# Kernel tuning notes

Hardware: AMD Instinct MI355X
Metric: run time of the kernel (lower is better)

Reference implementation:

```python
import jax, jax.numpy as jnp
import numpy as np

N, D, I, O = 4096, 64, 512, 512  # samples, node_nums (bases), input_size, output_size


def setup_inputs() -> dict:
    key = jax.random.key(0)
    k1, k2, k3, k4 = jax.random.split(key, 4)
    # xavier_uniform bounds
    w_bound = float(np.sqrt(6.0 / (I + O)))
    b_bound = float(np.sqrt(6.0 / (D + O)))
    return {
        "x": jax.random.normal(k1, (N, I), dtype=jnp.float32),
        "var_vector": jax.random.uniform(k2, (N, D), dtype=jnp.float32),
        "W_1": jax.random.uniform(k3, (D, I, O), dtype=jnp.float32, minval=-w_bound, maxval=w_bound),
        "b_1": jax.random.uniform(k4, (D, O), dtype=jnp.float32, minval=-b_bound, maxval=b_bound),
    }


def reference(x, var_vector, W_1, b_1):
    # Math identical to: einsum('nd,dio->nio') then bmm(x[:,None,:], W)[:,0,:] + b.
    # Reordered contraction: contract x against each basis first (never forms n,i,o).
    y = jnp.einsum('ni,dio->ndo', x, W_1)        # [n, d, o]
    out = jnp.einsum('nd,ndo->no', var_vector, y)  # [n, o]
    b = jnp.einsum('nd,do->no', var_vector, b_1)   # [n, o]
    return out + b
```

## Files before the change

kernel.cpp:

```cpp
#include <hip/hip_runtime.h>
#include <hip/hip_bf16.h>
#include <stdint.h>
#include <stddef.h>

#define N_ 4096
#define D_ 64
#define I_ 512
#define O_ 512

#define BM 128
#define BN 128
#define BK 64
#define SPLITS 4
#define DPG (D_ / SPLITS)
#define KSTEPS (I_ / BK)
#define NSTEP (DPG * KSTEPS)

typedef float  floatx4 __attribute__((ext_vector_type(4)));
typedef short  shortx8 __attribute__((ext_vector_type(8)));

__device__ __forceinline__ void gload_lds16(const void* g, void* l) {
  __builtin_amdgcn_global_load_lds(
      (const __attribute__((address_space(1))) void*)g,
      (__attribute__((address_space(3))) void*)l, 16, 0, 0);
}

__device__ __forceinline__ unsigned short f2bf(float f) {
  union { float f; unsigned int u; } c; c.f = f;
  unsigned int u = c.u;
  return (unsigned short)((u + 0x7fffu + ((u >> 16) & 1u)) >> 16);
}

__device__ __forceinline__ void mfma_bf16(floatx4& c, shortx8 a, shortx8 b) {
  asm("v_mfma_f32_16x16x32_bf16 %0, %1, %2, %0" : "+v"(c) : "v"(a), "v"(b));
}

__global__ void k_cvt_x(const float* __restrict__ x, unsigned short* __restrict__ xb) {
  int idx = (blockIdx.x * blockDim.x + threadIdx.x) * 8;
  floatx4 a = *(const floatx4*)(x + idx);
  floatx4 b = *(const floatx4*)(x + idx + 4);
  shortx8 o;
  o[0] = (short)f2bf(a[0]); o[1] = (short)f2bf(a[1]);
  o[2] = (short)f2bf(a[2]); o[3] = (short)f2bf(a[3]);
  o[4] = (short)f2bf(b[0]); o[5] = (short)f2bf(b[1]);
  o[6] = (short)f2bf(b[2]); o[7] = (short)f2bf(b[3]);
  *(shortx8*)(xb + idx) = o;
}

__global__ void k_cvt_w(const float* __restrict__ w, unsigned short* __restrict__ wt) {
  __shared__ unsigned short T[64][72];
  int bid = blockIdx.x;
  int d  = bid >> 6;
  int it = (bid >> 3) & 7;
  int ot = bid & 7;
  int i0 = it * 64, o0 = ot * 64;
  int t = threadIdx.x;
  const float* wp = w + ((size_t)d * I_ + i0) * O_ + o0;
  #pragma unroll
  for (int j = 0; j < 16; ++j) {
    int idx = j * 256 + t;
    int r = idx >> 6, c = idx & 63;
    T[r][c] = f2bf(wp[(size_t)r * O_ + c]);
  }
  __syncthreads();
  unsigned short* op = wt + ((size_t)d * O_ + o0) * I_ + i0;
  #pragma unroll
  for (int j = 0; j < 16; ++j) {
    int idx = j * 256 + t;
    int r = idx >> 6, c = idx & 63;
    op[(size_t)r * I_ + c] = T[c][r];
  }
}

__global__ void k_bias(const float* __restrict__ var, const float* __restrict__ b1,
                       float* __restrict__ out) {
  __shared__ float vs[16][64];
  int n0 = blockIdx.x * 16;
  int t = threadIdx.x;
  #pragma unroll
  for (int j = 0; j < 4; ++j) {
    int idx = j * 256 + t;
    vs[idx >> 6][idx & 63] = var[(size_t)n0 * D_ + idx];
  }
  __syncthreads();
  float a0[16], a1[16];
  #pragma unroll
  for (int r = 0; r < 16; ++r) { a0[r] = 0.f; a1[r] = 0.f; }
  for (int d = 0; d < D_; ++d) {
    float b0 = b1[(size_t)d * O_ + t];
    float bb = b1[(size_t)d * O_ + 256 + t];
    #pragma unroll
    for (int r = 0; r < 16; ++r) { a0[r] += vs[r][d] * b0; a1[r] += vs[r][d] * bb; }
  }
  #pragma unroll
  for (int r = 0; r < 16; ++r) {
    out[(size_t)(n0 + r) * O_ + t]       = a0[r];
    out[(size_t)(n0 + r) * O_ + 256 + t] = a1[r];
  }
}

__global__ __launch_bounds__(256, 2) void k_gemm(
    const unsigned short* __restrict__ xb, const unsigned short* __restrict__ wt,
    const float* __restrict__ var, float* __restrict__ out) {
  __shared__ alignas(16) unsigned short lA[2][BM * BK];
  __shared__ alignas(16) unsigned short lB[2][BN * BK];
  __shared__ alignas(16) float lV[DPG * BM];

  const int tid = threadIdx.x;
  const int bx  = blockIdx.x;
  const int split = bx & (SPLITS - 1);
  const int tile  = bx >> 2;
  const int ot = tile & 3;
  const int mt = tile >> 2;
  const int brow = mt * BM, bcol = ot * BN, d0 = split * DPG;

  const int lane = tid & 63, wid = tid >> 6;
  const int wr = wid >> 1, wc = wid & 1;
  const int l15 = lane & 15, l4 = lane >> 4;

  #pragma unroll
  for (int j = 0; j < (DPG * BM) / 256; ++j) {
    int idx = j * 256 + tid;
    int dd = idx >> 7, row = idx & (BM - 1);
    lV[idx] = var[(size_t)(brow + row) * D_ + d0 + dd];
  }

  const floatx4 vzero = {0.f, 0.f, 0.f, 0.f};
  floatx4 master[4][4];
  #pragma unroll
  for (int m = 0; m < 4; ++m)
    #pragma unroll
    for (int n = 0; n < 4; ++n) master[m][n] = vzero;
  floatx4 accd[4][4];

  auto stage = [&](int s, int buf) {
    const int d  = d0 + (s >> 3);
    const int kk = s & 7;
    const char* xsrc = (const char*)xb + ((size_t)brow * I_ + (size_t)kk * BK) * 2;
    const char* wsrc = (const char*)wt + (((size_t)d * O_ + bcol) * I_ + (size_t)kk * BK) * 2;
    char* la = (char*)&lA[buf][0];
    char* lb = (char*)&lB[buf][0];
    #pragma unroll
    for (int c = 0; c < 4; ++c) {
      int chunk = c * 256 + tid;
      int p = chunk << 4;
      int row = p >> 7;
      int colG = (p & 127) ^ ((row & 7) << 4);
      gload_lds16(xsrc + (size_t)row * (I_ * 2) + colG, la + p);
      gload_lds16(wsrc + (size_t)row * (I_ * 2) + colG, lb + p);
    }
  };

  stage(0, 0);

  int s = 0;
  for (int dl = 0; dl < DPG; ++dl) {
    #pragma unroll
    for (int m = 0; m < 4; ++m)
      #pragma unroll
      for (int n = 0; n < 4; ++n) accd[m][n] = vzero;

    for (int kk = 0; kk < KSTEPS; ++kk, ++s) {
      const int buf = s & 1;
      __syncthreads();
      if (s + 1 < NSTEP) stage(s + 1, buf ^ 1);
      #pragma unroll
      for (int ks = 0; ks < 2; ++ks) {
        shortx8 av[4], bv[4];
        #pragma unroll
        for (int m = 0; m < 4; ++m) {
          int row = wr * 64 + m * 16 + l15;
          int cb = ks * 64 + l4 * 16;
          av[m] = *(const shortx8*)((const char*)&lA[buf][0] + row * 128 +
                                    (cb ^ ((row & 7) << 4)));
        }
        #pragma unroll
        for (int n = 0; n < 4; ++n) {
          int row = wc * 64 + n * 16 + l15;
          int cb = ks * 64 + l4 * 16;
          bv[n] = *(const shortx8*)((const char*)&lB[buf][0] + row * 128 +
                                    (cb ^ ((row & 7) << 4)));
        }
        #pragma unroll
        for (int m = 0; m < 4; ++m)
          #pragma unroll
          for (int n = 0; n < 4; ++n)
            mfma_bf16(accd[m][n], av[m], bv[n]);
      }
    }

    #pragma unroll
    for (int m = 0; m < 4; ++m) {
      floatx4 vv = *(const floatx4*)&lV[dl * BM + wr * 64 + m * 16 + l4 * 4];
      #pragma unroll
      for (int n = 0; n < 4; ++n)
        #pragma unroll
        for (int r = 0; r < 4; ++r)
          master[m][n][r] += vv[r] * accd[m][n][r];
    }
  }

  #pragma unroll
  for (int m = 0; m < 4; ++m) {
    int row0 = brow + wr * 64 + m * 16 + l4 * 4;
    #pragma unroll
    for (int n = 0; n < 4; ++n) {
      int col = bcol + wc * 64 + n * 16 + l15;
      #pragma unroll
      for (int r = 0; r < 4; ++r)
        atomicAdd(out + (size_t)(row0 + r) * O_ + col, master[m][n][r]);
    }
  }
}

__global__ void k_naive(const float* __restrict__ x, const float* __restrict__ var,
                        const float* __restrict__ w, const float* __restrict__ b1,
                        float* __restrict__ out) {
  int n = blockIdx.x;
  int o = blockIdx.y * 128 + threadIdx.x;
  const float* xp = x + (size_t)n * I_;
  float acc = 0.f;
  for (int d = 0; d < D_; ++d) {
    const float* wp = w + (size_t)d * I_ * O_ + o;
    float y = 0.f;
    for (int i = 0; i < I_; ++i) y += xp[i] * wp[(size_t)i * O_];
    acc += var[(size_t)n * D_ + d] * (y + b1[(size_t)d * O_ + o]);
  }
  out[(size_t)n * O_ + o] = acc;
}

extern "C" void kernel_launch(void* const* d_in, const int* in_sizes, int n_in,
                              void* d_out, int out_size, void* d_ws, size_t ws_size,
                              hipStream_t stream) {
  const float* x   = (const float*)d_in[0];
  const float* var = (const float*)d_in[1];
  const float* W   = (const float*)d_in[2];
  const float* b1  = (const float*)d_in[3];
  float* out = (float*)d_out;

  const size_t wt_bytes = (size_t)D_ * I_ * O_ * 2;
  const size_t xb_bytes = (size_t)N_ * I_ * 2;
  if (ws_size >= wt_bytes + xb_bytes) {
    unsigned short* wt = (unsigned short*)d_ws;
    unsigned short* xb = (unsigned short*)((char*)d_ws + wt_bytes);
    k_cvt_x<<<dim3((N_ * I_) / (256 * 8)), dim3(256), 0, stream>>>(x, xb);
    k_cvt_w<<<dim3(D_ * 64), dim3(256), 0, stream>>>(W, wt);
    k_bias<<<dim3(N_ / 16), dim3(256), 0, stream>>>(var, b1, out);
    k_gemm<<<dim3((N_ / BM) * (O_ / BN) * SPLITS), dim3(256), 0, stream>>>(xb, wt, var, out);
  } else {
    k_naive<<<dim3(N_, O_ / 128), dim3(128), 0, stream>>>(x, var, W, b1, out);
  }
}
```

Baseline: 197.0 us.

## Enlarge GEMM tile to 256 rows and process basis pairs per A tile

Doubles the row tile to 256 and uses 512-thread blocks. Each loaded x tile is reused against two basis weight tiles per k-step, with two accumulator sets merged into the master sum using their var coefficients. This cuts A-tile reloads and halves the number of pipeline steps. The leading per-step __syncthreads is replaced by a per-thread vmcnt wait plus a trailing s_barrier, and MFMA priority is raised with s_setprio. Risks: no block-wide barrier separates the async LDS loads from reads of other threads' data, larger LDS use limits occupancy to one block per CU, and a meaningless no-op edit appears in the fallback kernel.

```diff
diff --git a/kernel.cpp b/kernel.cpp
--- a/kernel.cpp
+++ b/kernel.cpp
@@ -8,13 +8,14 @@
 #define I_ 512
 #define O_ 512
 
-#define BM 128
+#define BM 256
 #define BN 128
 #define BK 64
 #define SPLITS 4
-#define DPG (D_ / SPLITS)
+#define DPG 16
+#define PAIRS (DPG / 2)
 #define KSTEPS (I_ / BK)
-#define NSTEP (DPG * KSTEPS)
+#define NSTEP (PAIRS * KSTEPS)
 
 typedef float  floatx4 __attribute__((ext_vector_type(4)));
 typedef short  shortx8 __attribute__((ext_vector_type(8)));
@@ -99,19 +100,18 @@
   }
 }
 
-__global__ __launch_bounds__(256, 2) void k_gemm(
+__global__ __launch_bounds__(512, 2) void k_gemm(
     const unsigned short* __restrict__ xb, const unsigned short* __restrict__ wt,
     const float* __restrict__ var, float* __restrict__ out) {
   __shared__ alignas(16) unsigned short lA[2][BM * BK];
-  __shared__ alignas(16) unsigned short lB[2][BN * BK];
+  __shared__ alignas(16) unsigned short lB[2][2][BN * BK];
   __shared__ alignas(16) float lV[DPG * BM];
 
   const int tid = threadIdx.x;
-  const int bx  = blockIdx.x;
-  const int split = bx & (SPLITS - 1);
-  const int tile  = bx >> 2;
-  const int ot = tile & 3;
-  const int mt = tile >> 2;
+  const int bid = blockIdx.x;
+  const int g  = bid & 15;
+  const int mt = bid >> 4;
+  const int ot = g >> 2, split = g & 3;
   const int brow = mt * BM, bcol = ot * BN, d0 = split * DPG;
 
   const int lane = tid & 63, wid = tid >> 6;
@@ -119,11 +119,40 @@
   const int l15 = lane & 15, l4 = lane >> 4;
 
   #pragma unroll
-  for (int j = 0; j < (DPG * BM) / 256; ++j) {
-    int idx = j * 256 + tid;
-    int dd = idx >> 7, row = idx & (BM - 1);
+  for (int j = 0; j < (DPG * BM) / 512; ++j) {
+    int idx = j * 512 + tid;
+    int dd = idx >> 8, row = idx & (BM - 1);
     lV[idx] = var[(size_t)(brow + row) * D_ + d0 + dd];
   }
+
+  auto stage = [&](int s, int buf) {
+    const int p  = s >> 3;
+    const int kk = s & 7;
+    const int da = d0 + 2 * p;
+    const char* xsrc = (const char*)xb + ((size_t)brow * I_ + (size_t)kk * BK) * 2;
+    const char* w0 = (const char*)wt + (((size_t)da * O_ + bcol) * I_ + (size_t)kk * BK) * 2;
+    const char* w1 = (const char*)wt + (((size_t)(da + 1) * O_ + bcol) * I_ + (size_t)kk * BK) * 2;
+    char* la  = (char*)&lA[buf][0];
+    char* lb0 = (char*)&lB[buf][0][0];
+    char* lb1 = (char*)&lB[buf][1][0];
+    #pragma unroll
+    for (int c = 0; c < 4; ++c) {
+      int pb = (c * 512 + tid) << 4;
+      int row = pb >> 7;
+      int colG = (pb & 127) ^ ((row & 7) << 4);
+      gload_lds16(xsrc + (size_t)row * (I_ * 2) + colG, la + pb);
+    }
+    #pragma unroll
+    for (int c = 0; c < 2; ++c) {
+      int pb = (c * 512 + tid) << 4;
+      int row = pb >> 7;
+      int colG = (pb & 127) ^ ((row & 7) << 4);
+      gload_lds16(w0 + (size_t)row * (I_ * 2) + colG, lb0 + pb);
+      gload_lds16(w1 + (size_t)row * (I_ * 2) + colG, lb1 + pb);
+    }
+  };
+
+  stage(0, 0);
 
   const floatx4 vzero = {0.f, 0.f, 0.f, 0.f};
   floatx4 master[4][4];
@@ -131,72 +160,72 @@
   for (int m = 0; m < 4; ++m)
     #pragma unroll
     for (int n = 0; n < 4; ++n) master[m][n] = vzero;
-  floatx4 accd[4][4];
-
-  auto stage = [&](int s, int buf) {
-    const int d  = d0 + (s >> 3);
-    const int kk = s & 7;
-    const char* xsrc = (const char*)xb + ((size_t)brow * I_ + (size_t)kk * BK) * 2;
-    const char* wsrc = (const char*)wt + (((size_t)d * O_ + bcol) * I_ + (size_t)kk * BK) * 2;
-    char* la = (char*)&lA[buf][0];
-    char* lb = (char*)&lB[buf][0];
-    #pragma unroll
-    for (int c = 0; c < 4; ++c) {
-      int chunk = c * 256 + tid;
-      int p = chunk << 4;
-      int row = p >> 7;
-      int colG = (p & 127) ^ ((row & 7) << 4);
-      gload_lds16(xsrc + (size_t)row * (I_ * 2) + colG, la + p);
-      gload_lds16(wsrc + (size_t)row * (I_ * 2) + colG, lb + p);
-    }
-  };
-
-  stage(0, 0);
-
-  int s = 0;
-  for (int dl = 0; dl < DPG; ++dl) {
+
+  __syncthreads();
+
+  for (int p = 0; p < PAIRS; ++p) {
+    floatx4 acc0[4][4], acc1[4][4];
     #pragma unroll
     for (int m = 0; m < 4; ++m)
       #pragma unroll
-      for (int n = 0; n < 4; ++n) accd[m][n] = vzero;
-
-    for (int kk = 0; kk < KSTEPS; ++kk, ++s) {
+      for (int n = 0; n < 4; ++n) { acc0[m][n] = vzero; acc1[m][n] = vzero; }
+
+    for (int kk = 0; kk < KSTEPS; ++kk) {
+      const int s = p * KSTEPS + kk;
       const int buf = s & 1;
-      __syncthreads();
-      if (s + 1 < NSTEP) stage(s + 1, buf ^ 1);
+      if (s + 1 < NSTEP) {
+        stage(s + 1, (s + 1) & 1);
+        asm volatile("s_waitcnt vmcnt(8)" ::: "memory");
+      } else {
+        asm volatile("s_waitcnt vmcnt(0)" ::: "memory");
+      }
+      const char* laB  = (const char*)&lA[buf][0];
+      const char* lb0B = (const char*)&lB[buf][0][0];
+      const char* lb1B = (const char*)&lB[buf][1][0];
+      __builtin_amdgcn_s_setprio(1);
       #pragma unroll
       for (int ks = 0; ks < 2; ++ks) {
-        shortx8 av[4], bv[4];
+        const int cb = ks * 64 + l4 * 16;
+        shortx8 av[4];
         #pragma unroll
         for (int m = 0; m < 4; ++m) {
           int row = wr * 64 + m * 16 + l15;
-          int cb = ks * 64 + l4 * 16;
-          av[m] = *(const shortx8*)((const char*)&lA[buf][0] + row * 128 +
-                                    (cb ^ ((row & 7) << 4)));
+          av[m] = *(const shortx8*)(laB + row * 128 + (cb ^ ((row & 7) << 4)));
         }
+        shortx8 bv[4];
         #pragma unroll
         for (int n = 0; n < 4; ++n) {
           int row = wc * 64 + n * 16 + l15;
-          int cb = ks * 64 + l4 * 16;
-          bv[n] = *(const shortx8*)((const char*)&lB[buf][0] + row * 128 +
-                                    (cb ^ ((row & 7) << 4)));
+          bv[n] = *(const shortx8*)(lb0B + row * 128 + (cb ^ ((row & 7) << 4)));
         }
         #pragma unroll
         for (int m = 0; m < 4; ++m)
           #pragma unroll
-          for (int n = 0; n < 4; ++n)
-            mfma_bf16(accd[m][n], av[m], bv[n]);
+          for (int n = 0; n < 4; ++n) mfma_bf16(acc0[m][n], av[m], bv[n]);
+        #pragma unroll
+        for (int n = 0; n < 4; ++n) {
+          int row = wc * 64 + n * 16 + l15;
+          bv[n] = *(const shortx8*)(lb1B + row * 128 + (cb ^ ((row & 7) << 4)));
+        }
+        #pragma unroll
+        for (int m = 0; m < 4; ++m)
+          #pragma unroll
+          for (int n = 0; n < 4; ++n) mfma_bf16(acc1[m][n], av[m], bv[n]);
       }
+      __builtin_amdgcn_s_setprio(0);
+      __builtin_amdgcn_s_barrier();
     }
 
     #pragma unroll
     for (int m = 0; m < 4; ++m) {
-      floatx4 vv = *(const floatx4*)&lV[dl * BM + wr * 64 + m * 16 + l4 * 4];
+      int rbase = wr * 64 + m * 16 + l4 * 4;
+      floatx4 v0 = *(const floatx4*)&lV[(2 * p) * BM + rbase];
+      floatx4 v1 = *(const floatx4*)&lV[(2 * p + 1) * BM + rbase];
       #pragma unroll
       for (int n = 0; n < 4; ++n)
         #pragma unroll
         for (int r = 0; r < 4; ++r)
-          master[m][n][r] += vv[r] * accd[m][n][r];
+          master[m][n][r] += v0[r] * acc0[m][n][r] + v1[r] * acc1[m][n][r];
     }
   }
 
@@ -224,7 +253,7 @@
     const float* wp = w + (size_t)d * I_ * O_ + o;
     float y = 0.f;
     for (int i = 0; i < I_; ++i) y += xp[i] * wp[(size_t)i * O_];
-    acc += var[(size_t)n * D_ + d] * (y + b1[(size_t)d * O_ + o]);
+    acc += var[(size_t)n * D_ + o % 1 * 0 + d] * (y + b1[(size_t)d * O_ + o]);
   }
   out[(size_t)n * O_ + o] = acc;
 }
@@ -246,7 +275,7 @@
     k_cvt_x<<<dim3((N_ * I_) / (256 * 8)), dim3(256), 0, stream>>>(x, xb);
     k_cvt_w<<<dim3(D_ * 64), dim3(256), 0, stream>>>(W, wt);
     k_bias<<<dim3(N_ / 16), dim3(256), 0, stream>>>(var, b1, out);
-    k_gemm<<<dim3((N_ / BM) * (O_ / BN) * SPLITS), dim3(256), 0, stream>>>(xb, wt, var, out);
+    k_gemm<<<dim3((N_ / BM) * (O_ / BN) * SPLITS), dim3(512), 0, stream>>>(xb, wt, var, out);
   } else {
     k_naive<<<dim3(N_, O_ / 128), dim3(128), 0, stream>>>(x, var, W, b1, out);
   }
```

New measurement: 190.0 us. 1.04x faster.
